# Kernel optimization log

Hardware: AMD Instinct MI355X
Metric: run time of the kernel (lower is better)

Reference implementation:

```python
import jax, jax.numpy as jnp
import numpy as np

B, T, DIM = 4, 1024, 2048
H, KVH = 16, 4
HD = DIM // H          # 128
G = H // KVH           # GQA group size = 4


def setup_inputs() -> dict:
    key = jax.random.key(0)
    ks = jax.random.split(key, 4)
    s = 1.0 / np.sqrt(DIM)
    x = jax.random.normal(ks[0], (B, T, DIM), jnp.float32)
    Wq = jax.random.normal(ks[1], (DIM, DIM), jnp.float32) * s
    Wkv = jax.random.normal(ks[2], (DIM, 2 * KVH * HD), jnp.float32) * s
    Wo = jax.random.normal(ks[3], (DIM, DIM), jnp.float32) * s
    # RoPE tables (theta=10000, half-split / rotate-half convention)
    inv_freq = 1.0 / (10000.0 ** (np.arange(0, HD, 2, dtype=np.float64) / HD))
    freqs = np.outer(np.arange(T, dtype=np.float64), inv_freq)  # [T, HD/2]
    cos = jnp.asarray(np.cos(freqs), jnp.float32)
    sin = jnp.asarray(np.sin(freqs), jnp.float32)
    return {"x": x, "Wq": Wq, "Wkv": Wkv, "Wo": Wo, "cos": cos, "sin": sin}


def _rope(u, cos, sin):
    # u: [B,T,heads,HD]; cos/sin: [T, HD/2]
    u1, u2 = jnp.split(u, 2, axis=-1)
    c = cos[None, :, None, :]
    s = sin[None, :, None, :]
    return jnp.concatenate([u1 * c - u2 * s, u1 * s + u2 * c], axis=-1)


def reference(x, Wq, Wkv, Wo, cos, sin):
    Bs, Ts, C = x.shape
    q = (x @ Wq).reshape(Bs, Ts, H, HD)
    kv = (x @ Wkv).reshape(Bs, Ts, 2, KVH, HD)
    k, v = kv[:, :, 0], kv[:, :, 1]
    q = _rope(q, cos, sin)
    k = _rope(k, cos, sin)
    # GQA without materializing repeated K/V: fold group dim into q
    qg = q.reshape(Bs, Ts, KVH, G, HD)
    scores = jnp.einsum('bqhgd,bkhd->bhgqk', qg, k) / np.float32(np.sqrt(HD))
    causal = jnp.tril(jnp.ones((Ts, Ts), bool))
    neg = jnp.finfo(scores.dtype).min
    scores = jnp.where(causal, scores, neg)
    att = jax.nn.softmax(scores, axis=-1)
    out = jnp.einsum('bhgqk,bkhd->bqhgd', att, v).reshape(Bs, Ts, C)
    return out @ Wo
```

## Files before the change

### kernel.cpp

```cpp
#include <hip/hip_runtime.h>

typedef unsigned short u16;
typedef unsigned int u32;
typedef __bf16 bf16x8 __attribute__((ext_vector_type(8)));
typedef float f32x4 __attribute__((ext_vector_type(4)));

#define BB   4
#define TT   1024
#define CDIM 2048
#define NH   16
#define NKV  4
#define HDIM 128

__device__ __forceinline__ float b2f(u16 u) {
    union { u32 i; float f; } x; x.i = ((u32)u) << 16; return x.f;
}
__device__ __forceinline__ u16 f2b(float f) {
    union { float f; u32 i; } x; x.f = f;
    u32 r = (x.i + 0x7fffu + ((x.i >> 16) & 1u)) >> 16;
    return (u16)r;
}
__device__ __forceinline__ void async16(const void* g, void* l) {
    __builtin_amdgcn_global_load_lds((const __attribute__((address_space(1))) void*)g,
                                     (__attribute__((address_space(3))) void*)l, 16, 0, 0);
}

__device__ __forceinline__ bool wave_is_f32(const u16* xp) {
    u16 v = xp[(threadIdx.x & 63) * 2];
    int e = (v >> 7) & 0xFF;
    bool bad = (v != 0) && (e < 90 || e > 160);
    return __popcll(__ballot(bad)) > 16;
}

__global__ __launch_bounds__(256) void pre_k(const void* __restrict__ x,
                                             const void* __restrict__ Wq,
                                             const void* __restrict__ Wkv,
                                             const void* __restrict__ Wo,
                                             u16* __restrict__ xb,
                                             u16* __restrict__ csb,
                                             u16* __restrict__ snb,
                                             u16* __restrict__ WqkvT,
                                             u16* __restrict__ WoT,
                                             const void* __restrict__ cs,
                                             const void* __restrict__ sn) {
    const bool f32m = wave_is_f32((const u16*)x);
    int bid = blockIdx.x;
    if (bid < 8320) {
        const void* src; u16* dst; int i;
        if (bid < 8192)      { src = x;  dst = xb;  i = bid * 256 + threadIdx.x; }
        else if (bid < 8256) { src = cs; dst = csb; i = (bid - 8192) * 256 + threadIdx.x; }
        else                 { src = sn; dst = snb; i = (bid - 8256) * 256 + threadIdx.x; }
        union { u16 u[4]; ushort4 v; } o;
        if (f32m) {
            float4 f = ((const float4*)src)[i];
            o.u[0] = f2b(f.x); o.u[1] = f2b(f.y); o.u[2] = f2b(f.z); o.u[3] = f2b(f.w);
        } else {
            o.v = ((const ushort4*)src)[i];
        }
        ((ushort4*)dst)[i] = o.v;
        return;
    }
    __shared__ alignas(16) u16 tile[64 * 65];
    int t = bid - 8320;
    const void* W; u16* WT; int rows, cols, bx, by;
    if (t < 1024)      { W = Wq;  WT = WqkvT;                    rows = 2048; cols = 2048; bx = t & 31;  by = t >> 5; }
    else if (t < 1536) { int l = t - 1024; W = Wkv; WT = WqkvT + (long)2048 * 2048; rows = 2048; cols = 1024; bx = l & 15; by = l >> 4; }
    else               { int l = t - 1536; W = Wo;  WT = WoT;  rows = 2048; cols = 2048; bx = l & 31;   by = l >> 5; }
    const int r0 = by * 64, c0 = bx * 64;
#pragma unroll
    for (int i = 0; i < 16; i++) {
        int c = threadIdx.x + i * 256;
        int rr = c >> 6, cc = c & 63;
        long idx = (long)(r0 + rr) * cols + c0 + cc;
        tile[rr * 65 + cc] = f32m ? f2b(((const float*)W)[idx]) : ((const u16*)W)[idx];
    }
    __syncthreads();
#pragma unroll
    for (int i = 0; i < 16; i++) {
        int c = threadIdx.x + i * 256;
        int rr = c >> 6, cc = c & 63;
        WT[(long)(c0 + rr) * rows + r0 + cc] = tile[cc * 65 + rr];
    }
}

__global__ __launch_bounds__(256) void gemm_bt(const u16* __restrict__ A,
                                               const u16* __restrict__ Bt,
                                               void* __restrict__ C,
                                               int M, int N, int Kd,
                                               const u16* __restrict__ xprobe) {
    __shared__ alignas(16) u16 As[128 * 32];
    __shared__ alignas(16) u16 Bs[128 * 32];
    const bool f32m = (xprobe != nullptr) && wave_is_f32(xprobe);
    const int tid = threadIdx.x;
    const int w = tid >> 6, lane = tid & 63;
    const int wm = w >> 1, wn = w & 1;
    const int l16 = lane & 15, quad = lane >> 4;
    const int bm = blockIdx.y, bn = blockIdx.x;
    const long arow0 = (long)bm * 128;
    const long brow0 = (long)bn * 128;
    const int srow = lane >> 2;
    const int schunk = lane & 3;

    f32x4 acc[4][4];
#pragma unroll
    for (int i = 0; i < 4; i++)
#pragma unroll
        for (int j = 0; j < 4; j++) acc[i][j] = {0.f, 0.f, 0.f, 0.f};

    for (int k0 = 0; k0 < Kd; k0 += 32) {
        __syncthreads();
#pragma unroll
        for (int j = 0; j < 2; j++) {
            int r0 = w * 32 + j * 16;
            const u16* gA = A + (arow0 + r0 + srow) * Kd + k0 + schunk * 8;
            async16(gA, &As[r0 * 32]);
            const u16* gB = Bt + (brow0 + r0 + srow) * Kd + k0 + schunk * 8;
            async16(gB, &Bs[r0 * 32]);
        }
        __syncthreads();
        bf16x8 af[4], bfr[4];
#pragma unroll
        for (int mt = 0; mt < 4; mt++)
            af[mt] = *(const bf16x8*)&As[(wm * 64 + mt * 16 + l16) * 32 + quad * 8];
#pragma unroll
        for (int nt = 0; nt < 4; nt++)
            bfr[nt] = *(const bf16x8*)&Bs[(wn * 64 + nt * 16 + l16) * 32 + quad * 8];
#pragma unroll
        for (int mt = 0; mt < 4; mt++)
#pragma unroll
            for (int nt = 0; nt < 4; nt++)
                acc[mt][nt] = __builtin_amdgcn_mfma_f32_16x16x32_bf16(
                    af[mt], bfr[nt], acc[mt][nt], 0, 0, 0);
    }
#pragma unroll
    for (int mt = 0; mt < 4; mt++) {
#pragma unroll
        for (int nt = 0; nt < 4; nt++) {
            int col = bn * 128 + wn * 64 + nt * 16 + l16;
#pragma unroll
            for (int r = 0; r < 4; r++) {
                long row = bm * 128 + wm * 64 + mt * 16 + quad * 4 + r;
                if (f32m) ((float*)C)[row * N + col] = acc[mt][nt][r];
                else      ((u16*)C)[row * N + col] = f2b(acc[mt][nt][r]);
            }
        }
    }
}

__global__ __launch_bounds__(256) void prep_k(const u16* __restrict__ QKVraw,
                                              const u16* __restrict__ cs,
                                              const u16* __restrict__ sn,
                                              u16* __restrict__ Qr,
                                              u16* __restrict__ Kr,
                                              u16* __restrict__ Vt) {
    int bid = blockIdx.x;
    if (bid < 16384) {
        int idx = bid * 256 + threadIdx.x;
        int d = idx & 63;
        int t = (idx >> 6) & (TT - 1);
        int bh = idx >> 16;
        long src = ((long)((bh >> 4) * TT + t)) * 3072 + (bh & 15) * HDIM;
        float u1 = b2f(QKVraw[src + d]), u2 = b2f(QKVraw[src + d + 64]);
        float c = b2f(cs[t * 64 + d]), s = b2f(sn[t * 64 + d]);
        long dst = ((long)bh * TT + t) * HDIM;
        Qr[dst + d] = f2b(u1 * c - u2 * s);
        Qr[dst + d + 64] = f2b(u1 * s + u2 * c);
    } else if (bid < 20480) {
        int idx = (bid - 16384) * 256 + threadIdx.x;
        int d = idx & 63;
        int t = (idx >> 6) & (TT - 1);
        int bk = idx >> 16;
        long src = ((long)((bk >> 2) * TT + t)) * 3072 + 2048 + (bk & 3) * HDIM;
        float u1 = b2f(QKVraw[src + d]), u2 = b2f(QKVraw[src + d + 64]);
        float c = b2f(cs[t * 64 + d]), s = b2f(sn[t * 64 + d]);
        long dst = ((long)bk * TT + t) * HDIM;
        Kr[dst + d] = f2b(u1 * c - u2 * s);
        Kr[dst + d + 64] = f2b(u1 * s + u2 * c);
    } else {
        int idx = (bid - 20480) * 256 + threadIdx.x;
        int t = idx & (TT - 1);
        int d = (idx >> 10) & (HDIM - 1);
        int bk = idx >> 17;
        Vt[idx] = QKVraw[((long)(bk >> 2) * TT + t) * 3072 + 2560 + (bk & 3) * HDIM + d];
    }
}

__global__ __launch_bounds__(256) void attn_kernel(const u16* __restrict__ Q,
                                                   const u16* __restrict__ Kr,
                                                   const u16* __restrict__ Vt,
                                                   u16* __restrict__ O) {
    __shared__ alignas(16) u16 Ks[2][64 * 128];
    __shared__ alignas(16) u16 Vts[2][128 * 64];
    __shared__ alignas(16) u16 Ps[64 * 88];

    const int tid = threadIdx.x, w = tid >> 6, lane = tid & 63;
    const int l16 = lane & 15, quad = lane >> 4;
    const float scale2 = 0.08838834764831845f * 1.4426950408889634f;

#pragma unroll 1
    for (int it = 0; it < 2; it++) {
        const int j = it ? (1023 - (int)blockIdx.x) : (int)blockIdx.x;
        const int qt = 15 - (j >> 6);
        const int bh = j & 63;
        const int b = bh >> 4, h = bh & 15;
        const int kvh = h >> 2;
        const long qrow0 = (long)bh * TT + qt * 64;
        const long krow0 = (long)(b * NKV + kvh) * TT;
        const long vbase = ((long)(b * NKV + kvh) * HDIM) * TT;

        __syncthreads();

#pragma unroll
        for (int i = 0; i < 4; i++) {
            int slot0 = (w * 4 + i) * 64;
            int slot = slot0 + lane;
            int row = slot >> 4, cp = slot & 15;
            int cg = (cp & 8) | ((cp ^ row) & 7);
            async16(Q + (qrow0 + row) * HDIM + cg * 8, &Ks[0][slot0 * 8]);
        }
        asm volatile("s_waitcnt vmcnt(0)" ::: "memory");
        bf16x8 qf[4];
        {
            const int Rq = w * 16 + l16;
#pragma unroll
            for (int ds = 0; ds < 4; ds++) {
                int c = ds * 4 + quad;
                qf[ds] = *(const bf16x8*)&Ks[0][Rq * 128 + ((c & 8) | ((c ^ Rq) & 7)) * 8];
            }
        }
        asm volatile("s_waitcnt lgkmcnt(0)" ::: "memory");

#pragma unroll
        for (int i = 0; i < 4; i++) {
            int slot0 = (w * 4 + i) * 64;
            int slot = slot0 + lane;
            int row = slot >> 4, cp = slot & 15;
            int cg = (cp & 8) | ((cp ^ row) & 7);
            async16(Kr + (krow0 + row) * HDIM + cg * 8, &Ks[0][slot0 * 8]);
        }
#pragma unroll
        for (int i = 0; i < 4; i++) {
            int slot0 = (w * 4 + i) * 64;
            int slot = slot0 + lane;
            int row = slot >> 3, cp = slot & 7;
            int cg = cp ^ (row & 7);
            async16(Vt + vbase + (long)row * TT + cg * 8, &Vts[0][slot0 * 8]);
        }
        if (qt >= 1) {
#pragma unroll
            for (int i = 0; i < 4; i++) {
                int slot0 = (w * 4 + i) * 64;
                int slot = slot0 + lane;
                int row = slot >> 4, cp = slot & 15;
                int cg = (cp & 8) | ((cp ^ row) & 7);
                async16(Kr + (krow0 + 64 + row) * HDIM + cg * 8, &Ks[1][slot0 * 8]);
            }
#pragma unroll
            for (int i = 0; i < 4; i++) {
                int slot0 = (w * 4 + i) * 64;
                int slot = slot0 + lane;
                int row = slot >> 3, cp = slot & 7;
                int cg = cp ^ (row & 7);
                async16(Vt + vbase + (long)row * TT + 64 + cg * 8, &Vts[1][slot0 * 8]);
            }
            asm volatile("s_waitcnt vmcnt(8)" ::: "memory");
        } else {
            asm volatile("s_waitcnt vmcnt(0)" ::: "memory");
        }
        asm volatile("s_barrier" ::: "memory");

        f32x4 o[8];
#pragma unroll
        for (int i = 0; i < 8; i++) o[i] = {0.f, 0.f, 0.f, 0.f};
        float m_i = -1.0e30f, l_i = 0.f;
        const int qg = qt * 64 + w * 16 + l16;

#pragma unroll 1
        for (int kt = 0; kt <= qt; kt++) {
            const int cur = kt & 1;
            const u16* ksb = Ks[cur];
            const u16* vsb = Vts[cur];

            f32x4 s[4];
#pragma unroll
            for (int nt = 0; nt < 4; nt++) s[nt] = {0.f, 0.f, 0.f, 0.f};
#pragma unroll
            for (int ds = 0; ds < 4; ds++) {
                int c = ds * 4 + quad;
#pragma unroll
                for (int nt = 0; nt < 4; nt++) {
                    int Rk = nt * 16 + l16;
                    bf16x8 ak = *(const bf16x8*)&ksb[Rk * 128 + ((c & 8) | ((c ^ Rk) & 7)) * 8];
                    s[nt] = __builtin_amdgcn_mfma_f32_16x16x32_bf16(ak, qf[ds], s[nt], 0, 0, 0);
                }
            }

            float p[4][4];
            float mx = -1.0e30f;
            if (kt == qt) {
#pragma unroll
                for (int nt = 0; nt < 4; nt++)
#pragma unroll
                    for (int r = 0; r < 4; r++) {
                        int kcol = kt * 64 + nt * 16 + quad * 4 + r;
                        float v = (kcol <= qg) ? (float)s[nt][r] * scale2 : -1.0e30f;
                        p[nt][r] = v;
                        mx = fmaxf(mx, v);
                    }
            } else {
#pragma unroll
                for (int nt = 0; nt < 4; nt++)
#pragma unroll
                    for (int r = 0; r < 4; r++) {
                        float v = (float)s[nt][r] * scale2;
                        p[nt][r] = v;
                        mx = fmaxf(mx, v);
                    }
            }
            mx = fmaxf(mx, __shfl_xor(mx, 16));
            mx = fmaxf(mx, __shfl_xor(mx, 32));
            float mnew = fmaxf(m_i, mx);
            float alpha = exp2f(m_i - mnew);
            float rs = 0.f;
#pragma unroll
            for (int nt = 0; nt < 4; nt++)
#pragma unroll
                for (int r = 0; r < 4; r++) {
                    float e = exp2f(p[nt][r] - mnew);
                    p[nt][r] = e;
                    rs += e;
                }
            rs += __shfl_xor(rs, 16);
            rs += __shfl_xor(rs, 32);
            l_i = l_i * alpha + rs;

            u32* Psw = (u32*)Ps;
            int pb = (w * 16 + l16) * 44 + quad * 2;
#pragma unroll
            for (int nt = 0; nt < 4; nt++) {
                u32 lo = (u32)f2b(p[nt][0]) | ((u32)f2b(p[nt][1]) << 16);
                u32 hi = (u32)f2b(p[nt][2]) | ((u32)f2b(p[nt][3]) << 16);
                Psw[pb + nt * 8]     = lo;
                Psw[pb + nt * 8 + 1] = hi;
            }
            if (__ballot(mnew != m_i) != 0ULL) {
#pragma unroll
                for (int n8 = 0; n8 < 8; n8++)
#pragma unroll
                    for (int r = 0; r < 4; r++) o[n8][r] *= alpha;
            }
            m_i = mnew;

            asm volatile("s_waitcnt lgkmcnt(0)" ::: "memory");

#pragma unroll
            for (int ks = 0; ks < 2; ks++) {
                bf16x8 bp = *(const bf16x8*)&Ps[(w * 16 + l16) * 88 + ks * 32 + quad * 8];
#pragma unroll
                for (int n8 = 0; n8 < 8; n8++) {
                    int Rv = n8 * 16 + l16;
                    int c = ks * 4 + quad;
                    bf16x8 av = *(const bf16x8*)&vsb[Rv * 64 + (c ^ (Rv & 7)) * 8];
                    o[n8] = __builtin_amdgcn_mfma_f32_16x16x32_bf16(av, bp, o[n8], 0, 0, 0);
                }
            }

            if (kt == qt) break;

            asm volatile("s_waitcnt lgkmcnt(0)" ::: "memory");
            asm volatile("s_barrier" ::: "memory");
            if (kt + 2 <= qt) {
                const int nk = kt + 2;
#pragma unroll
                for (int i = 0; i < 4; i++) {
                    int slot0 = (w * 4 + i) * 64;
                    int slot = slot0 + lane;
                    int row = slot >> 4, cp = slot & 15;
                    int cg = (cp & 8) | ((cp ^ row) & 7);
                    async16(Kr + (krow0 + nk * 64 + row) * HDIM + cg * 8, &Ks[cur][slot0 * 8]);
                }
#pragma unroll
                for (int i = 0; i < 4; i++) {
                    int slot0 = (w * 4 + i) * 64;
                    int slot = slot0 + lane;
                    int row = slot >> 3, cp = slot & 7;
                    int cg = cp ^ (row & 7);
                    async16(Vt + vbase + (long)row * TT + nk * 64 + cg * 8, &Vts[cur][slot0 * 8]);
                }
                asm volatile("s_waitcnt vmcnt(8)" ::: "memory");
            } else {
                asm volatile("s_waitcnt vmcnt(0)" ::: "memory");
            }
            asm volatile("s_barrier" ::: "memory");
        }

        float inv = 1.0f / l_i;
        long obase = ((long)(b * TT + qg)) * CDIM + h * HDIM;
#pragma unroll
        for (int n8 = 0; n8 < 8; n8++) {
            ushort4 st;
            st.x = f2b(o[n8][0] * inv);
            st.y = f2b(o[n8][1] * inv);
            st.z = f2b(o[n8][2] * inv);
            st.w = f2b(o[n8][3] * inv);
            *(ushort4*)&O[obase + n8 * 16 + quad * 4] = st;
        }
    }
}

extern "C" void kernel_launch(void* const* d_in, const int* in_sizes, int n_in,
                              void* d_out, int out_size, void* d_ws, size_t ws_size,
                              hipStream_t stream) {
    const void* x   = d_in[0];
    const void* Wq  = d_in[1];
    const void* Wkv = d_in[2];
    const void* Wo  = d_in[3];
    const void* cs  = d_in[4];
    const void* sn  = d_in[5];

    char* ws = (char*)d_ws;
    const size_t NEED = 105119748;
    if (ws_size < NEED) return;

    u16* WqkvT = (u16*)(ws + 0);
    u16* WoT   = (u16*)(ws + 12582912);
    u16* QKVraw= (u16*)(ws + 20971520);
    u16* Qr    = (u16*)(ws + 46137344);
    u16* Kr    = (u16*)(ws + 62914560);
    u16* Vt    = (u16*)(ws + 67108864);
    u16* ATT   = (u16*)(ws + 71303168);
    u16* xb    = (u16*)(ws + 88080384);
    u16* csb   = (u16*)(ws + 104857600);
    u16* snb   = (u16*)(ws + 104988672);

    pre_k<<<10880, 256, 0, stream>>>(x, Wq, Wkv, Wo, xb, csb, snb, WqkvT, WoT, cs, sn);

    gemm_bt<<<dim3(24, 32), 256, 0, stream>>>(xb, WqkvT, QKVraw, 4096, 3072, 2048, nullptr);

    prep_k<<<28672, 256, 0, stream>>>(QKVraw, csb, snb, Qr, Kr, Vt);

    attn_kernel<<<512, 256, 0, stream>>>(Qr, Kr, Vt, ATT);

    gemm_bt<<<dim3(16, 32), 256, 0, stream>>>(ATT, WoT, d_out, 4096, 2048, 2048, (const u16*)x);
}
```

Before: 328.1 us.

## Fuse RoPE into QKV GEMM epilogue and enlarge attention query tile to 128

The QKV projection GEMM now applies RoPE in its epilogue and writes rotated Q and K directly in head-major layout, with each block covering one full head so both rotation halves are in registers. V goes to a compact buffer and is transposed by a separate tiled LDS kernel. This removes the large QKVraw intermediate and the elementwise prep pass. The attention kernel now processes 128 query rows per block (two 16-row halves per wave), so each K/V tile load serves twice as many queries, at the cost of more registers and half as many blocks.

```diff
diff --git a/kernel.cpp b/kernel.cpp
--- a/kernel.cpp
+++ b/kernel.cpp
@@ -83,6 +83,95 @@
     }
 }
 
+__global__ __launch_bounds__(256) void gemm_qkv(const u16* __restrict__ A,
+                                                const u16* __restrict__ Bt,
+                                                u16* __restrict__ Qr,
+                                                u16* __restrict__ Kr,
+                                                u16* __restrict__ Vraw,
+                                                const u16* __restrict__ csb,
+                                                const u16* __restrict__ snb) {
+    __shared__ alignas(16) u16 As[128 * 32];
+    __shared__ alignas(16) u16 Bs[128 * 32];
+    const int tid = threadIdx.x;
+    const int w = tid >> 6, lane = tid & 63;
+    const int l16 = lane & 15, quad = lane >> 4;
+    const int bm = blockIdx.y, bn = blockIdx.x;
+    const long arow0 = (long)bm * 128;
+    const long brow0 = (long)bn * 128;
+    const int srow = lane >> 2;
+    const int schunk = lane & 3;
+    const int Kd = 2048;
+
+    f32x4 acc[2][8];
+#pragma unroll
+    for (int i = 0; i < 2; i++)
+#pragma unroll
+        for (int j = 0; j < 8; j++) acc[i][j] = {0.f, 0.f, 0.f, 0.f};
+
+    for (int k0 = 0; k0 < Kd; k0 += 32) {
+        __syncthreads();
+#pragma unroll
+        for (int j = 0; j < 2; j++) {
+            int r0 = w * 32 + j * 16;
+            const u16* gA = A + (arow0 + r0 + srow) * Kd + k0 + schunk * 8;
+            async16(gA, &As[r0 * 32]);
+            const u16* gB = Bt + (brow0 + r0 + srow) * Kd + k0 + schunk * 8;
+            async16(gB, &Bs[r0 * 32]);
+        }
+        __syncthreads();
+        bf16x8 af[2], bfr[8];
+#pragma unroll
+        for (int mt = 0; mt < 2; mt++)
+            af[mt] = *(const bf16x8*)&As[(w * 32 + mt * 16 + l16) * 32 + quad * 8];
+#pragma unroll
+        for (int nt = 0; nt < 8; nt++)
+            bfr[nt] = *(const bf16x8*)&Bs[(nt * 16 + l16) * 32 + quad * 8];
+#pragma unroll
+        for (int mt = 0; mt < 2; mt++)
+#pragma unroll
+            for (int nt = 0; nt < 8; nt++)
+                acc[mt][nt] = __builtin_amdgcn_mfma_f32_16x16x32_bf16(
+                    af[mt], bfr[nt], acc[mt][nt], 0, 0, 0);
+    }
+
+    if (bn < 20) {
+        u16* dst = (bn < 16) ? Qr : Kr;
+        const int head = (bn < 16) ? bn : (bn - 16);
+        const int hmul = (bn < 16) ? 16 : 4;
+#pragma unroll
+        for (int mt = 0; mt < 2; mt++) {
+#pragma unroll
+            for (int nt = 0; nt < 4; nt++) {
+                int d = nt * 16 + l16;
+#pragma unroll
+                for (int r = 0; r < 4; r++) {
+                    int t = bm * 128 + w * 32 + mt * 16 + quad * 4 + r;
+                    int tt = t & 1023, bb = t >> 10;
+                    float c = b2f(csb[tt * 64 + d]);
+                    float s = b2f(snb[tt * 64 + d]);
+                    float u1 = acc[mt][nt][r], u2 = acc[mt][nt + 4][r];
+                    long base = ((long)((bb * hmul + head) * 1024 + tt)) * 128;
+                    dst[base + d] = f2b(u1 * c - u2 * s);
+                    dst[base + d + 64] = f2b(u1 * s + u2 * c);
+                }
+            }
+        }
+    } else {
+        const int v0 = (bn - 20) * 128;
+#pragma unroll
+        for (int mt = 0; mt < 2; mt++)
+#pragma unroll
+            for (int nt = 0; nt < 8; nt++) {
+                int col = nt * 16 + l16;
+#pragma unroll
+                for (int r = 0; r < 4; r++) {
+                    int t = bm * 128 + w * 32 + mt * 16 + quad * 4 + r;
+                    Vraw[(long)t * 512 + v0 + col] = f2b(acc[mt][nt][r]);
+                }
+            }
+    }
+}
+
 __global__ __launch_bounds__(256) void gemm_bt(const u16* __restrict__ A,
                                                const u16* __restrict__ Bt,
                                                void* __restrict__ C,
@@ -147,41 +236,26 @@
     }
 }
 
-__global__ __launch_bounds__(256) void prep_k(const u16* __restrict__ QKVraw,
-                                              const u16* __restrict__ cs,
-                                              const u16* __restrict__ sn,
-                                              u16* __restrict__ Qr,
-                                              u16* __restrict__ Kr,
-                                              u16* __restrict__ Vt) {
+__global__ __launch_bounds__(256) void vt2_k(const u16* __restrict__ Vraw,
+                                             u16* __restrict__ Vt) {
+    __shared__ alignas(16) u16 tile[64 * 65];
     int bid = blockIdx.x;
-    if (bid < 16384) {
-        int idx = bid * 256 + threadIdx.x;
-        int d = idx & 63;
-        int t = (idx >> 6) & (TT - 1);
-        int bh = idx >> 16;
-        long src = ((long)((bh >> 4) * TT + t)) * 3072 + (bh & 15) * HDIM;
-        float u1 = b2f(QKVraw[src + d]), u2 = b2f(QKVraw[src + d + 64]);
-        float c = b2f(cs[t * 64 + d]), s = b2f(sn[t * 64 + d]);
-        long dst = ((long)bh * TT + t) * HDIM;
-        Qr[dst + d] = f2b(u1 * c - u2 * s);
-        Qr[dst + d + 64] = f2b(u1 * s + u2 * c);
-    } else if (bid < 20480) {
-        int idx = (bid - 16384) * 256 + threadIdx.x;
-        int d = idx & 63;
-        int t = (idx >> 6) & (TT - 1);
-        int bk = idx >> 16;
-        long src = ((long)((bk >> 2) * TT + t)) * 3072 + 2048 + (bk & 3) * HDIM;
-        float u1 = b2f(QKVraw[src + d]), u2 = b2f(QKVraw[src + d + 64]);
-        float c = b2f(cs[t * 64 + d]), s = b2f(sn[t * 64 + d]);
-        long dst = ((long)bk * TT + t) * HDIM;
-        Kr[dst + d] = f2b(u1 * c - u2 * s);
-        Kr[dst + d + 64] = f2b(u1 * s + u2 * c);
-    } else {
-        int idx = (bid - 20480) * 256 + threadIdx.x;
-        int t = idx & (TT - 1);
-        int d = (idx >> 10) & (HDIM - 1);
-        int bk = idx >> 17;
-        Vt[idx] = QKVraw[((long)(bk >> 2) * TT + t) * 3072 + 2560 + (bk & 3) * HDIM + d];
+    int bkv = bid >> 5;
+    int dx = (bid >> 4) & 1, tx = bid & 15;
+    int bb = bkv >> 2, kvh = bkv & 3;
+#pragma unroll
+    for (int i = 0; i < 16; i++) {
+        int c = threadIdx.x + i * 256;
+        int rr = c >> 6, cc = c & 63;
+        tile[rr * 65 + cc] =
+            Vraw[((long)(bb * 1024 + tx * 64 + rr)) * 512 + kvh * 128 + dx * 64 + cc];
+    }
+    __syncthreads();
+#pragma unroll
+    for (int i = 0; i < 16; i++) {
+        int c = threadIdx.x + i * 256;
+        int rr = c >> 6, cc = c & 63;
+        Vt[((long)bkv * 128 + dx * 64 + rr) * 1024 + tx * 64 + cc] = tile[cc * 65 + rr];
     }
 }
 
@@ -191,7 +265,7 @@
                                                    u16* __restrict__ O) {
     __shared__ alignas(16) u16 Ks[2][64 * 128];
     __shared__ alignas(16) u16 Vts[2][128 * 64];
-    __shared__ alignas(16) u16 Ps[64 * 88];
+    __shared__ alignas(16) u16 Ps[128 * 88];
 
     const int tid = threadIdx.x, w = tid >> 6, lane = tid & 63;
     const int l16 = lane & 15, quad = lane >> 4;
@@ -199,61 +273,50 @@
 
 #pragma unroll 1
     for (int it = 0; it < 2; it++) {
-        const int j = it ? (1023 - (int)blockIdx.x) : (int)blockIdx.x;
-        const int qt = 15 - (j >> 6);
+        const int j = it ? (511 - (int)blockIdx.x) : (int)blockIdx.x;
+        const int qt2 = 7 - (j >> 6);
         const int bh = j & 63;
         const int b = bh >> 4, h = bh & 15;
         const int kvh = h >> 2;
-        const long qrow0 = (long)bh * TT + qt * 64;
+        const int nkt = 2 * qt2 + 2;
+        const long qrow0 = (long)bh * TT + qt2 * 128;
         const long krow0 = (long)(b * NKV + kvh) * TT;
         const long vbase = ((long)(b * NKV + kvh) * HDIM) * TT;
 
         __syncthreads();
 
 #pragma unroll
-        for (int i = 0; i < 4; i++) {
-            int slot0 = (w * 4 + i) * 64;
-            int slot = slot0 + lane;
-            int row = slot >> 4, cp = slot & 15;
-            int cg = (cp & 8) | ((cp ^ row) & 7);
-            async16(Q + (qrow0 + row) * HDIM + cg * 8, &Ks[0][slot0 * 8]);
+        for (int i = 0; i < 8; i++) {
+            int grb = w * 32 + i * 4;
+            int buf = w >> 1;
+            int lrb = grb & 63;
+            int gr = grb + (lane >> 4);
+            int cp = lane & 15;
+            int cg = (cp & 8) | ((cp ^ gr) & 7);
+            async16(Q + (qrow0 + gr) * HDIM + cg * 8, &Ks[buf][lrb * 128]);
         }
         asm volatile("s_waitcnt vmcnt(0)" ::: "memory");
-        bf16x8 qf[4];
-        {
-            const int Rq = w * 16 + l16;
+        bf16x8 qf[2][4];
+#pragma unroll
+        for (int hf = 0; hf < 2; hf++) {
+            int Rq = (w & 1) * 32 + hf * 16 + l16;
 #pragma unroll
             for (int ds = 0; ds < 4; ds++) {
                 int c = ds * 4 + quad;
-                qf[ds] = *(const bf16x8*)&Ks[0][Rq * 128 + ((c & 8) | ((c ^ Rq) & 7)) * 8];
-            }
-        }
-        asm volatile("s_waitcnt lgkmcnt(0)" ::: "memory");
-
-#pragma unroll
-        for (int i = 0; i < 4; i++) {
-            int slot0 = (w * 4 + i) * 64;
-            int slot = slot0 + lane;
-            int row = slot >> 4, cp = slot & 15;
-            int cg = (cp & 8) | ((cp ^ row) & 7);
-            async16(Kr + (krow0 + row) * HDIM + cg * 8, &Ks[0][slot0 * 8]);
-        }
-#pragma unroll
-        for (int i = 0; i < 4; i++) {
-            int slot0 = (w * 4 + i) * 64;
-            int slot = slot0 + lane;
-            int row = slot >> 3, cp = slot & 7;
-            int cg = cp ^ (row & 7);
-            async16(Vt + vbase + (long)row * TT + cg * 8, &Vts[0][slot0 * 8]);
-        }
-        if (qt >= 1) {
+                qf[hf][ds] = *(const bf16x8*)&Ks[w >> 1][Rq * 128 + ((c & 8) | ((c ^ Rq) & 7)) * 8];
+            }
+        }
+        __syncthreads();
+
+#pragma unroll
+        for (int kt0 = 0; kt0 < 2; kt0++) {
 #pragma unroll
             for (int i = 0; i < 4; i++) {
                 int slot0 = (w * 4 + i) * 64;
                 int slot = slot0 + lane;
                 int row = slot >> 4, cp = slot & 15;
                 int cg = (cp & 8) | ((cp ^ row) & 7);
-                async16(Kr + (krow0 + 64 + row) * HDIM + cg * 8, &Ks[1][slot0 * 8]);
+                async16(Kr + (krow0 + kt0 * 64 + row) * HDIM + cg * 8, &Ks[kt0][slot0 * 8]);
             }
 #pragma unroll
             for (int i = 0; i < 4; i++) {
@@ -261,29 +324,31 @@
                 int slot = slot0 + lane;
                 int row = slot >> 3, cp = slot & 7;
                 int cg = cp ^ (row & 7);
-                async16(Vt + vbase + (long)row * TT + 64 + cg * 8, &Vts[1][slot0 * 8]);
-            }
-            asm volatile("s_waitcnt vmcnt(8)" ::: "memory");
-        } else {
-            asm volatile("s_waitcnt vmcnt(0)" ::: "memory");
-        }
+                async16(Vt + vbase + (long)row * TT + kt0 * 64 + cg * 8, &Vts[kt0][slot0 * 8]);
+            }
+        }
+        asm volatile("s_waitcnt vmcnt(8)" ::: "memory");
         asm volatile("s_barrier" ::: "memory");
 
-        f32x4 o[8];
-#pragma unroll
-        for (int i = 0; i < 8; i++) o[i] = {0.f, 0.f, 0.f, 0.f};
-        float m_i = -1.0e30f, l_i = 0.f;
-        const int qg = qt * 64 + w * 16 + l16;
+        f32x4 o[2][8];
+#pragma unroll
+        for (int hf = 0; hf < 2; hf++)
+#pragma unroll
+            for (int i = 0; i < 8; i++) o[hf][i] = {0.f, 0.f, 0.f, 0.f};
+        float m_i[2] = {-1.0e30f, -1.0e30f}, l_i[2] = {0.f, 0.f};
+        const int qg0 = qt2 * 128 + w * 32 + l16;
 
 #pragma unroll 1
-        for (int kt = 0; kt <= qt; kt++) {
+        for (int kt = 0; kt < nkt; kt++) {
             const int cur = kt & 1;
             const u16* ksb = Ks[cur];
             const u16* vsb = Vts[cur];
 
-            f32x4 s[4];
-#pragma unroll
-            for (int nt = 0; nt < 4; nt++) s[nt] = {0.f, 0.f, 0.f, 0.f};
+            f32x4 s[2][4];
+#pragma unroll
+            for (int hf = 0; hf < 2; hf++)
+#pragma unroll
+                for (int nt = 0; nt < 4; nt++) s[hf][nt] = {0.f, 0.f, 0.f, 0.f};
 #pragma unroll
             for (int ds = 0; ds < 4; ds++) {
                 int c = ds * 4 + quad;
@@ -291,85 +356,85 @@
                 for (int nt = 0; nt < 4; nt++) {
                     int Rk = nt * 16 + l16;
                     bf16x8 ak = *(const bf16x8*)&ksb[Rk * 128 + ((c & 8) | ((c ^ Rk) & 7)) * 8];
-                    s[nt] = __builtin_amdgcn_mfma_f32_16x16x32_bf16(ak, qf[ds], s[nt], 0, 0, 0);
-                }
-            }
-
-            float p[4][4];
-            float mx = -1.0e30f;
-            if (kt == qt) {
+                    s[0][nt] = __builtin_amdgcn_mfma_f32_16x16x32_bf16(ak, qf[0][ds], s[0][nt], 0, 0, 0);
+                    s[1][nt] = __builtin_amdgcn_mfma_f32_16x16x32_bf16(ak, qf[1][ds], s[1][nt], 0, 0, 0);
+                }
+            }
+
+            const bool need_mask = (kt >= 2 * qt2);
+            float alpha[2];
+#pragma unroll
+            for (int hf = 0; hf < 2; hf++) {
+                const int qg = qg0 + hf * 16;
+                float p[4][4];
+                float mx = -1.0e30f;
 #pragma unroll
                 for (int nt = 0; nt < 4; nt++)
 #pragma unroll
                     for (int r = 0; r < 4; r++) {
-                        int kcol = kt * 64 + nt * 16 + quad * 4 + r;
-                        float v = (kcol <= qg) ? (float)s[nt][r] * scale2 : -1.0e30f;
+                        float v = (float)s[hf][nt][r] * scale2;
+                        if (need_mask) {
+                            int kg = kt * 64 + nt * 16 + quad * 4 + r;
+                            if (kg > qg) v = -1.0e30f;
+                        }
                         p[nt][r] = v;
                         mx = fmaxf(mx, v);
                     }
-            } else {
+                mx = fmaxf(mx, __shfl_xor(mx, 16));
+                mx = fmaxf(mx, __shfl_xor(mx, 32));
+                float mnew = fmaxf(m_i[hf], mx);
+                alpha[hf] = exp2f(m_i[hf] - mnew);
+                float rs = 0.f;
 #pragma unroll
                 for (int nt = 0; nt < 4; nt++)
 #pragma unroll
                     for (int r = 0; r < 4; r++) {
-                        float v = (float)s[nt][r] * scale2;
-                        p[nt][r] = v;
-                        mx = fmaxf(mx, v);
+                        float e = exp2f(p[nt][r] - mnew);
+                        p[nt][r] = e;
+                        rs += e;
                     }
-            }
-            mx = fmaxf(mx, __shfl_xor(mx, 16));
-            mx = fmaxf(mx, __shfl_xor(mx, 32));
-            float mnew = fmaxf(m_i, mx);
-            float alpha = exp2f(m_i - mnew);
-            float rs = 0.f;
-#pragma unroll
-            for (int nt = 0; nt < 4; nt++)
-#pragma unroll
-                for (int r = 0; r < 4; r++) {
-                    float e = exp2f(p[nt][r] - mnew);
-                    p[nt][r] = e;
-                    rs += e;
-                }
-            rs += __shfl_xor(rs, 16);
-            rs += __shfl_xor(rs, 32);
-            l_i = l_i * alpha + rs;
-
-            u32* Psw = (u32*)Ps;
-            int pb = (w * 16 + l16) * 44 + quad * 2;
-#pragma unroll
-            for (int nt = 0; nt < 4; nt++) {
-                u32 lo = (u32)f2b(p[nt][0]) | ((u32)f2b(p[nt][1]) << 16);
-                u32 hi = (u32)f2b(p[nt][2]) | ((u32)f2b(p[nt][3]) << 16);
-                Psw[pb + nt * 8]     = lo;
-                Psw[pb + nt * 8 + 1] = hi;
-            }
-            if (__ballot(mnew != m_i) != 0ULL) {
-#pragma unroll
-                for (int n8 = 0; n8 < 8; n8++)
-#pragma unroll
-                    for (int r = 0; r < 4; r++) o[n8][r] *= alpha;
-            }
-            m_i = mnew;
+                rs += __shfl_xor(rs, 16);
+                rs += __shfl_xor(rs, 32);
+                l_i[hf] = l_i[hf] * alpha[hf] + rs;
+                m_i[hf] = mnew;
+                u32* Psw = (u32*)Ps;
+                int pb = (w * 32 + hf * 16 + l16) * 44 + quad * 2;
+#pragma unroll
+                for (int nt = 0; nt < 4; nt++) {
+                    uint2 pk;
+                    pk.x = (u32)f2b(p[nt][0]) | ((u32)f2b(p[nt][1]) << 16);
+                    pk.y = (u32)f2b(p[nt][2]) | ((u32)f2b(p[nt][3]) << 16);
+                    *(uint2*)&Psw[pb + nt * 8] = pk;
+                }
+                if (__ballot(alpha[hf] != 1.0f) != 0ULL) {
+#pragma unroll
+                    for (int n8 = 0; n8 < 8; n8++)
+#pragma unroll
+                        for (int r = 0; r < 4; r++) o[hf][n8][r] *= alpha[hf];
+                }
+            }
 
             asm volatile("s_waitcnt lgkmcnt(0)" ::: "memory");
 
 #pragma unroll
             for (int ks = 0; ks < 2; ks++) {
-                bf16x8 bp = *(const bf16x8*)&Ps[(w * 16 + l16) * 88 + ks * 32 + quad * 8];
+                bf16x8 bp0 = *(const bf16x8*)&Ps[(w * 32 + l16) * 88 + ks * 32 + quad * 8];
+                bf16x8 bp1 = *(const bf16x8*)&Ps[(w * 32 + 16 + l16) * 88 + ks * 32 + quad * 8];
 #pragma unroll
                 for (int n8 = 0; n8 < 8; n8++) {
                     int Rv = n8 * 16 + l16;
                     int c = ks * 4 + quad;
                     bf16x8 av = *(const bf16x8*)&vsb[Rv * 64 + (c ^ (Rv & 7)) * 8];
-                    o[n8] = __builtin_amdgcn_mfma_f32_16x16x32_bf16(av, bp, o[n8], 0, 0, 0);
-                }
-            }
-
-            if (kt == qt) break;
+                    o[0][n8] = __builtin_amdgcn_mfma_f32_16x16x32_bf16(av, bp0, o[0][n8], 0, 0, 0);
+                    o[1][n8] = __builtin_amdgcn_mfma_f32_16x16x32_bf16(av, bp1, o[1][n8], 0, 0, 0);
+                }
+            }
+
+            if (kt == nkt - 1) break;
 
             asm volatile("s_waitcnt lgkmcnt(0)" ::: "memory");
             asm volatile("s_barrier" ::: "memory");
-            if (kt + 2 <= qt) {
+            if (kt + 2 < nkt) {
                 const int nk = kt + 2;
 #pragma unroll
                 for (int i = 0; i < 4; i++) {
@@ -394,16 +459,20 @@
             asm volatile("s_barrier" ::: "memory");
         }
 
-        float inv = 1.0f / l_i;
-        long obase = ((long)(b * TT + qg)) * CDIM + h * HDIM;
-#pragma unroll
-        for (int n8 = 0; n8 < 8; n8++) {
-            ushort4 st;
-            st.x = f2b(o[n8][0] * inv);
-            st.y = f2b(o[n8][1] * inv);
-            st.z = f2b(o[n8][2] * inv);
-            st.w = f2b(o[n8][3] * inv);
-            *(ushort4*)&O[obase + n8 * 16 + quad * 4] = st;
+#pragma unroll
+        for (int hf = 0; hf < 2; hf++) {
+            float inv = 1.0f / l_i[hf];
+            const int qg = qg0 + hf * 16;
+            long obase = ((long)(b * TT + qg)) * CDIM + h * HDIM;
+#pragma unroll
+            for (int n8 = 0; n8 < 8; n8++) {
+                ushort4 st;
+                st.x = f2b(o[hf][n8][0] * inv);
+                st.y = f2b(o[hf][n8][1] * inv);
+                st.z = f2b(o[hf][n8][2] * inv);
+                st.w = f2b(o[hf][n8][3] * inv);
+                *(ushort4*)&O[obase + n8 * 16 + quad * 4] = st;
+            }
         }
     }
 }
@@ -419,27 +488,27 @@
     const void* sn  = d_in[5];
 
     char* ws = (char*)d_ws;
-    const size_t NEED = 105119748;
+    const size_t NEED = 84148224;
     if (ws_size < NEED) return;
 
     u16* WqkvT = (u16*)(ws + 0);
     u16* WoT   = (u16*)(ws + 12582912);
-    u16* QKVraw= (u16*)(ws + 20971520);
-    u16* Qr    = (u16*)(ws + 46137344);
-    u16* Kr    = (u16*)(ws + 62914560);
-    u16* Vt    = (u16*)(ws + 67108864);
-    u16* ATT   = (u16*)(ws + 71303168);
-    u16* xb    = (u16*)(ws + 88080384);
-    u16* csb   = (u16*)(ws + 104857600);
-    u16* snb   = (u16*)(ws + 104988672);
+    u16* Qr    = (u16*)(ws + 20971520);
+    u16* Kr    = (u16*)(ws + 37748736);
+    u16* Vraw  = (u16*)(ws + 41943040);
+    u16* Vt    = (u16*)(ws + 46137344);
+    u16* ATT   = (u16*)(ws + 50331648);
+    u16* xb    = (u16*)(ws + 67108864);
+    u16* csb   = (u16*)(ws + 83886080);
+    u16* snb   = (u16*)(ws + 84017152);
 
     pre_k<<<10880, 256, 0, stream>>>(x, Wq, Wkv, Wo, xb, csb, snb, WqkvT, WoT, cs, sn);
 
-    gemm_bt<<<dim3(24, 32), 256, 0, stream>>>(xb, WqkvT, QKVraw, 4096, 3072, 2048, nullptr);
-
-    prep_k<<<28672, 256, 0, stream>>>(QKVraw, csb, snb, Qr, Kr, Vt);
-
-    attn_kernel<<<512, 256, 0, stream>>>(Qr, Kr, Vt, ATT);
+    gemm_qkv<<<dim3(24, 32), 256, 0, stream>>>(xb, WqkvT, Qr, Kr, Vraw, csb, snb);
+
+    vt2_k<<<512, 256, 0, stream>>>(Vraw, Vt);
+
+    attn_kernel<<<256, 256, 0, stream>>>(Qr, Kr, Vt, ATT);
 
     gemm_bt<<<dim3(16, 32), 256, 0, stream>>>(ATT, WoT, d_out, 4096, 2048, 2048, (const u16*)x);
 }
```

New measurement: 344.5 us. 1.05x slower.
